# Optimization experiments

Measured on AMD Instinct MI355X. Metric: run time of the kernel, lower is better.

The kernel has to match this reference:

```python
import jax, jax.numpy as jnp
import numpy as np

N, C, T = 8, 256, 512
H, KQ, OUT = 8, 256, 256
EPS = 1e-5


def sym_linear(x, w, stride):
    # w: (2, out_dim); circulant-grouped expansion to (2T, out_dim), then x @ cp
    out_dim = w.shape[1]
    idx = (jnp.arange(out_dim)[None, :] - jnp.arange(T)[:, None] * stride) % out_dim  # (T, out_dim)
    cp = w[:, idx].transpose(1, 0, 2).reshape(2 * T, out_dim)  # cat of rolled copies
    return x @ cp


def ln2d(x, g, b):
    # LayerNorm over last two dims (T, 2T) with affine params (T, 2T)
    mu = jnp.mean(x, axis=(-2, -1), keepdims=True)
    var = jnp.mean(jnp.square(x - mu), axis=(-2, -1), keepdims=True)
    return (x - mu) / jnp.sqrt(var + EPS) * g + b


def setup_inputs() -> dict:
    key = jax.random.key(0)
    ks = jax.random.split(key, 16)
    stdv = 1.0 / np.sqrt(2 * T)
    u = lambda k, shape, s: jax.random.uniform(k, shape, jnp.float32, -s, s)
    return {
        "x": jax.random.normal(ks[0], (N, C, T), jnp.float32),
        "Wq": u(ks[1], (KQ, C), 1.0 / np.sqrt(C)),
        "Wk": u(ks[2], (KQ, C), 1.0 / np.sqrt(C)),
        "Wv": u(ks[3], (OUT, C), 1.0 / np.sqrt(C)),
        "m1w0": u(ks[4], (2, 2 * T), stdv),
        "m2w0": u(ks[5], (2, 2 * T), stdv),
        "m1w1": u(ks[6], (2, 2 * T), stdv),
        "m2w1": u(ks[7], (2, T), stdv),
        "ln1g0": 1.0 + 0.1 * jax.random.normal(ks[8], (T, 2 * T), jnp.float32),
        "ln1b0": 0.1 * jax.random.normal(ks[9], (T, 2 * T), jnp.float32),
        "ln2g0": 1.0 + 0.1 * jax.random.normal(ks[10], (T, 2 * T), jnp.float32),
        "ln2b0": 0.1 * jax.random.normal(ks[11], (T, 2 * T), jnp.float32),
        "ln1g1": 1.0 + 0.1 * jax.random.normal(ks[12], (T, 2 * T), jnp.float32),
        "ln1b1": 0.1 * jax.random.normal(ks[13], (T, 2 * T), jnp.float32),
    }


def reference(x, Wq, Wk, Wv, m1w0, m2w0, m1w1, m2w1,
              ln1g0, ln1b0, ln2g0, ln2b0, ln1g1, ln1b1):
    dk = KQ // H
    q = jnp.einsum('oc,nct->not', Wq, x).reshape(N, H, dk, T).transpose(0, 1, 3, 2)  # (N,H,T,dk)
    k = jnp.einsum('oc,nct->not', Wk, x).reshape(N, H, dk, T)                        # (N,H,dk,T)
    v = jnp.einsum('oc,nct->not', Wv, x).reshape(N, H, OUT // H, T).transpose(0, 1, 3, 2)  # (N,H,T,dv)

    scores = jnp.einsum('nhtd,nhds->nhts', q, k) / np.sqrt(dk)  # (N,H,T,T)
    ar = jnp.arange(T, dtype=jnp.float32)
    pd = jnp.abs(ar[None, :] - ar[:, None]) / (T - 1)  # (T,T)
    p = jnp.stack([scores, jnp.broadcast_to(pd, scores.shape)], axis=-1)  # (N,H,T,T,2)
    p = p.reshape(N, H, T, 2 * T)

    def transpose_pairs(z):
        return z.reshape(N, H, T, T, 2).transpose(0, 1, 3, 2, 4)

    # mix block 0 (intermediate)
    p = ln2d(sym_linear(p, m1w0, 2), ln1g0, ln1b0)
    p = jax.nn.gelu(transpose_pairs(p), approximate=False).reshape(N, H, T, 2 * T)
    p = ln2d(sym_linear(p, m2w0, 2), ln2g0, ln2b0)
    p = jax.nn.gelu(transpose_pairs(p), approximate=False).reshape(N, H, T, 2 * T)

    # mix block 1 (final)
    p = ln2d(sym_linear(p, m1w1, 2), ln1g1, ln1b1)
    p = jax.nn.gelu(transpose_pairs(p), approximate=False).reshape(N, H, T, 2 * T)
    p = sym_linear(p, m2w1, 1)           # (N,H,T,T), out_roll_stride = T // T * 1
    p = p.transpose(0, 1, 3, 2)

    attn = jax.nn.softmax(p, axis=-1)
    out = jnp.einsum('nhts,nhsd->nhtd', attn, v)  # (N,H,T,dv)
    return out.transpose(0, 1, 3, 2).reshape(N, OUT, T)
```

## Files before the change

### kernel.cpp

```cpp
#include <hip/hip_runtime.h>
#include <hip/hip_bf16.h>
#include <math.h>

#define CDIM 256
#define TDIM 512
#define T2   1024
#define NB   64
#define MTOT 524288.0f

typedef __bf16 bf16x8 __attribute__((ext_vector_type(8)));
typedef float  f32x4  __attribute__((ext_vector_type(4)));

__device__ __forceinline__ ushort f2bf(float f) {
  union { float f; unsigned u; } v; v.f = f;
  unsigned r = v.u + 0x7fffu + ((v.u >> 16) & 1u);
  return (ushort)(r >> 16);
}
__device__ __forceinline__ float bf2f(ushort h) {
  union { unsigned u; float f; } v; v.u = ((unsigned)h) << 16;
  return v.f;
}
__device__ __forceinline__ float gelu_exact(float x) {
  return 0.5f * x * (1.0f + erff(x * 0.7071067811865475f));
}

#define TO_LDS(p)  ((__attribute__((address_space(3))) void*)(unsigned)(uintptr_t)(p))
#define TO_GLB(p)  ((const __attribute__((address_space(1))) void*)(uintptr_t)(p))
#define GLOAD_LDS16(g, l) __builtin_amdgcn_global_load_lds(TO_GLB(g), TO_LDS(l), 16, 0, 0)

#define BAR()    asm volatile("s_barrier" ::: "memory")
#define WAITL()  asm volatile("s_waitcnt lgkmcnt(0)" ::: "memory")
#define WAITV4() asm volatile("s_waitcnt vmcnt(4)" ::: "memory")
#define WAITV0() asm volatile("s_waitcnt vmcnt(0)" ::: "memory")

__global__ __launch_bounds__(256)
void proj_kernel(const float* __restrict__ x, const float* __restrict__ Wq,
                 const float* __restrict__ Wk, const float* __restrict__ Wv,
                 float* __restrict__ qp, float* __restrict__ kp, float* __restrict__ vp) {
  int t = blockIdx.x * 256 + threadIdx.x;
  int o = blockIdx.y;
  int n = blockIdx.z;
  const float* xn = x + (long)n * CDIM * TDIM;
  float aq = 0.f, ak = 0.f, av = 0.f;
  for (int c = 0; c < CDIM; ++c) {
    float xv = xn[c * TDIM + t];
    aq = fmaf(Wq[o * CDIM + c], xv, aq);
    ak = fmaf(Wk[o * CDIM + c], xv, ak);
    av = fmaf(Wv[o * CDIM + c], xv, av);
  }
  long idx = ((long)n * 256 + o) * TDIM + t;
  qp[idx] = aq; kp[idx] = ak; vp[idx] = av;
}

__global__ __launch_bounds__(256)
void build_cpt_kernel(const float* __restrict__ w, ushort* __restrict__ cpt,
                      int outdim, int stride) {
  int i = blockIdx.x * 256 + threadIdx.x;
  int o  = i >> 10;
  int kk = i & 1023;
  int s = kk >> 1, r = kk & 1;
  float v = w[r * outdim + ((o - s * stride) & (outdim - 1))];
  cpt[i] = f2bf(v);
}

__global__ __launch_bounds__(256)
void build_p0_kernel(const float* __restrict__ qp, const float* __restrict__ kp,
                     ushort* __restrict__ P) {
  int s = blockIdx.x * 256 + threadIdx.x;
  int t = blockIdx.y;
  int b = blockIdx.z;
  int n = b >> 3, h = b & 7;
  const float* qrow = qp + ((long)n * 256 + h * 32) * TDIM + t;
  const float* krow = kp + ((long)n * 256 + h * 32) * TDIM + s;
  float acc = 0.f;
#pragma unroll
  for (int d = 0; d < 32; ++d) acc = fmaf(qrow[d * TDIM], krow[d * TDIM], acc);
  acc *= 0.17677669529663687f;
  float pd = fabsf((float)(s - t)) * (1.0f / 511.0f);
  ushort2 pr; pr.x = f2bf(acc); pr.y = f2bf(pd);
  *(ushort2*)(P + (((long)b * TDIM + t) * T2 + 2 * s)) = pr;
}


#define LDS_BUF  65536
#define LDS_BOFF 32768

#define STAGE_A_(buf, h, kt) do { \
  const ushort* gA0_ = Ab + (long)((h)*128 +      sr0) * 1024 + (kt)*64 + slog8; \
  const ushort* gA1_ = Ab + (long)((h)*128 + 64 + sr0) * 1024 + (kt)*64 + slog8; \
  char* dA_ = ldsw + (size_t)(buf) * LDS_BUF + (h)*16384 + tid*16; \
  GLOAD_LDS16(gA0_, dA_); GLOAD_LDS16(gA1_, dA_ + 8192); } while(0)

#define STAGE_B_(buf, h, kt) do { \
  const ushort* gB0_ = Bb + (long)((h)*128 +      sr0) * 1024 + (kt)*64 + slog8; \
  const ushort* gB1_ = Bb + (long)((h)*128 + 64 + sr0) * 1024 + (kt)*64 + slog8; \
  char* dB_ = ldsw + (size_t)(buf) * LDS_BUF + LDS_BOFF + (h)*16384 + tid*16; \
  GLOAD_LDS16(gB0_, dB_); GLOAD_LDS16(gB1_, dB_ + 8192); } while(0)

#define LD_A_(buf, mh) do { \
  const char* aB_ = ldsc + (size_t)(buf) * LDS_BUF; \
  _Pragma("unroll") for (int mi = 0; mi < 4; ++mi) { \
    int ar_ = wm*128 + (mh)*64 + mi*16 + fr; \
    const char* rb_ = aB_ + ar_*128; int sw_ = (ar_&7)<<4; \
    af[mi][0] = *(const bf16x8*)(rb_ + ((fq*16) ^ sw_)); \
    af[mi][1] = *(const bf16x8*)(rb_ + ((64 + fq*16) ^ sw_)); \
  } } while(0)

#define LD_B_(dst, buf, nh) do { \
  const char* bB_ = ldsc + (size_t)(buf) * LDS_BUF + LDS_BOFF; \
  _Pragma("unroll") for (int ni = 0; ni < 2; ++ni) { \
    int br_ = wn*64 + (nh)*32 + ni*16 + fr; \
    const char* rb_ = bB_ + br_*128; int sw_ = (br_&7)<<4; \
    dst[ni][0] = *(const bf16x8*)(rb_ + ((fq*16) ^ sw_)); \
    dst[ni][1] = *(const bf16x8*)(rb_ + ((64 + fq*16) ^ sw_)); \
  } } while(0)

#define QUAD_(mh, nh, bfa) do { \
  __builtin_amdgcn_s_setprio(1); \
  _Pragma("unroll") for (int kk = 0; kk < 2; ++kk) \
  _Pragma("unroll") for (int mi = 0; mi < 4; ++mi) \
  _Pragma("unroll") for (int ni = 0; ni < 2; ++ni) \
    acc[(mh)*4+mi][(nh)*2+ni] = __builtin_amdgcn_mfma_f32_16x16x32_bf16( \
        af[mi][kk], bfa[ni][kk], acc[(mh)*4+mi][(nh)*2+ni], 0, 0, 0); \
  __builtin_amdgcn_s_setprio(0); } while(0)

template<bool FINAL>
__global__ __launch_bounds__(512, 2)
void gemm256_kernel(const ushort* __restrict__ A, long aStride,
                    const ushort* __restrict__ BT, long bStride,
                    void* __restrict__ Out, int ncols, float* __restrict__ stats) {
  __shared__ ushort lds[2][2][256 * 64];
  const int tid = threadIdx.x;
  const int bm = blockIdx.x, bn = blockIdx.y, b = blockIdx.z;
  const ushort* Ab = A  + (long)b * aStride + (long)bm * 256 * 1024;
  const ushort* Bb = BT + (long)b * bStride + (long)bn * 256 * 1024;
  const int lane = tid & 63;
  const int fr = lane & 15, fq = lane >> 4;
  const int wid = tid >> 6, wm = wid >> 2, wn = wid & 3;
  const int sr0 = tid >> 3;
  const int slog8 = ((tid & 7) ^ (sr0 & 7)) * 8;
  const char* ldsc = (const char*)&lds[0][0][0];
  char*       ldsw = (char*)&lds[0][0][0];

  f32x4 acc[8][4] = {};
  bf16x8 af[4][2], bf0[2][2], bf1[2][2];

  STAGE_B_(0, 0, 0); STAGE_B_(0, 1, 0);
  STAGE_A_(0, 0, 0); STAGE_A_(0, 1, 0);
  STAGE_B_(1, 0, 1); STAGE_B_(1, 1, 1);
  WAITV4();
  BAR();

  for (int i = 0; i < 8; ++i) {
    const int t1 = 2 * i + 1, t2 = 2 * i + 2, t3 = 2 * i + 3;
    const bool st = (i < 7);
    LD_A_(0, 0); LD_B_(bf0, 0, 0);
    STAGE_A_(1, 0, t1);
    BAR(); WAITL(); QUAD_(0, 0, bf0); BAR();

    LD_B_(bf1, 0, 1);
    STAGE_A_(1, 1, t1);
    BAR(); WAITL(); QUAD_(0, 1, bf1); BAR();

    LD_A_(0, 1);
    if (st) STAGE_B_(0, 0, t2);
    BAR(); WAITL(); QUAD_(1, 1, bf1); BAR();

    if (st) { STAGE_B_(0, 1, t2); WAITV4(); } else { WAITV0(); }
    BAR(); QUAD_(1, 0, bf0); BAR();

    LD_A_(1, 0); LD_B_(bf0, 1, 0);
    if (st) STAGE_A_(0, 0, t2);
    BAR(); WAITL(); QUAD_(0, 0, bf0); BAR();

    LD_B_(bf1, 1, 1);
    if (st) STAGE_A_(0, 1, t2);
    BAR(); WAITL(); QUAD_(0, 1, bf1); BAR();

    LD_A_(1, 1);
    if (st) STAGE_B_(1, 0, t3);
    BAR(); WAITL(); QUAD_(1, 1, bf1); BAR();

    if (st) { STAGE_B_(1, 1, t3); WAITV4(); }
    BAR(); QUAD_(1, 0, bf0); BAR();
  }

  const int r0 = bm * 256 + wm * 128;
  const int c0 = bn * 256 + wn * 64;
  if (!FINAL) {
    ushort* Yb = (ushort*)Out + (long)b * 512 * ncols;
    float s1 = 0.f, s2 = 0.f;
#pragma unroll
    for (int mi = 0; mi < 8; ++mi)
#pragma unroll
      for (int ni = 0; ni < 4; ++ni)
#pragma unroll
        for (int r = 0; r < 4; ++r) {
          float v = acc[mi][ni][r];
          s1 += v; s2 += v * v;
          int row = r0 + mi * 16 + fq * 4 + r;
          int col = c0 + ni * 16 + fr;
          Yb[(long)row * ncols + col] = f2bf(v);
        }
    __syncthreads();
    float* red = (float*)&lds[0][0][0];
    red[tid] = s1; red[tid + 512] = s2;
    __syncthreads();
    for (int off = 256; off > 0; off >>= 1) {
      if (tid < off) { red[tid] += red[tid + off]; red[512 + tid] += red[512 + tid + off]; }
      __syncthreads();
    }
    if (tid == 0) {
      atomicAdd(&stats[b * 2],     red[0]);
      atomicAdd(&stats[b * 2 + 1], red[512]);
    }
  } else {
    float* Lb = (float*)Out + (long)b * 512 * 512;
#pragma unroll
    for (int mi = 0; mi < 8; ++mi)
#pragma unroll
      for (int ni = 0; ni < 4; ++ni)
#pragma unroll
        for (int r = 0; r < 4; ++r) {
          int row = r0 + mi * 16 + fq * 4 + r;
          int col = c0 + ni * 16 + fr;
          Lb[(long)row * 512 + col] = acc[mi][ni][r];
        }
  }
}

__global__ __launch_bounds__(256)
void apply_kernel(const ushort* __restrict__ Y, const float* __restrict__ stats,
                  const float* __restrict__ g, const float* __restrict__ bia,
                  ushort* __restrict__ P) {
  __shared__ ushort2 tile[32][33];
  int ti = blockIdx.x;
  int si = blockIdx.y;
  int b  = blockIdx.z;
  float mu  = stats[b * 2] * (1.0f / MTOT);
  float var = stats[b * 2 + 1] * (1.0f / MTOT) - mu * mu;
  float rstd = rsqrtf(var + 1e-5f);
  int tx = threadIdx.x & 31, ty = threadIdx.x >> 5;
  const ushort* Yb = Y + (long)b * 512 * 1024;
#pragma unroll
  for (int i = 0; i < 4; ++i) {
    int t  = ti * 32 + ty + i * 8;
    int sp = si * 32 + tx;
    ushort2 yv = *(const ushort2*)(Yb + (long)t * 1024 + 2 * sp);
    float2 gv = *(const float2*)(g   + (long)t * 1024 + 2 * sp);
    float2 bv = *(const float2*)(bia + (long)t * 1024 + 2 * sp);
    float y0 = (bf2f(yv.x) - mu) * rstd * gv.x + bv.x;
    float y1 = (bf2f(yv.y) - mu) * rstd * gv.y + bv.y;
    ushort2 o; o.x = f2bf(gelu_exact(y0)); o.y = f2bf(gelu_exact(y1));
    tile[ty + i * 8][tx] = o;
  }
  __syncthreads();
  ushort* Pb = P + (long)b * 512 * 1024;
#pragma unroll
  for (int i = 0; i < 4; ++i) {
    int srow = si * 32 + ty + i * 8;
    int tcol = ti * 32 + tx;
    ushort2 v = tile[tx][ty + i * 8];
    *(ushort2*)(Pb + (long)srow * 1024 + 2 * tcol) = v;
  }
}

__global__ __launch_bounds__(256)
void softmax_kernel(float* __restrict__ L) {
  int wid = threadIdx.x >> 6, lane = threadIdx.x & 63;
  long row = (long)blockIdx.x * 4 + wid;
  float* Lr = L + row * 512;
  float4 a = *(float4*)(Lr + lane * 8);
  float4 c = *(float4*)(Lr + lane * 8 + 4);
  float m = fmaxf(fmaxf(fmaxf(a.x, a.y), fmaxf(a.z, a.w)),
                  fmaxf(fmaxf(c.x, c.y), fmaxf(c.z, c.w)));
  for (int off = 32; off > 0; off >>= 1) m = fmaxf(m, __shfl_xor(m, off, 64));
  a.x = expf(a.x - m); a.y = expf(a.y - m); a.z = expf(a.z - m); a.w = expf(a.w - m);
  c.x = expf(c.x - m); c.y = expf(c.y - m); c.z = expf(c.z - m); c.w = expf(c.w - m);
  float s = a.x + a.y + a.z + a.w + c.x + c.y + c.z + c.w;
  for (int off = 32; off > 0; off >>= 1) s += __shfl_xor(s, off, 64);
  float inv = 1.0f / s;
  a.x *= inv; a.y *= inv; a.z *= inv; a.w *= inv;
  c.x *= inv; c.y *= inv; c.z *= inv; c.w *= inv;
  *(float4*)(Lr + lane * 8) = a;
  *(float4*)(Lr + lane * 8 + 4) = c;
}

__global__ __launch_bounds__(256)
void av_kernel(const float* __restrict__ L, const float* __restrict__ vp,
               float* __restrict__ out) {
  __shared__ float vt[32 * 512];
  int bh = blockIdx.x;
  int at = blockIdx.y;
  int n = bh >> 3, h = bh & 7;
  const float* vsrc = vp + ((long)n * 256 + h * 32) * 512;
  for (int i = threadIdx.x; i < 32 * 512 / 4; i += 256)
    ((float4*)vt)[i] = ((const float4*)vsrc)[i];
  __syncthreads();
  int a  = at * 32 + (threadIdx.x & 31);
  int d0 = (threadIdx.x >> 5) * 4;
  const float* Lr = L + ((long)bh * 512 + a) * 512;
  float acc0 = 0.f, acc1 = 0.f, acc2 = 0.f, acc3 = 0.f;
  for (int bcol = 0; bcol < 512; ++bcol) {
    float p = Lr[bcol];
    acc0 = fmaf(p, vt[(d0 + 0) * 512 + bcol], acc0);
    acc1 = fmaf(p, vt[(d0 + 1) * 512 + bcol], acc1);
    acc2 = fmaf(p, vt[(d0 + 2) * 512 + bcol], acc2);
    acc3 = fmaf(p, vt[(d0 + 3) * 512 + bcol], acc3);
  }
  float* ob = out + ((long)n * 256 + h * 32) * 512;
  ob[(d0 + 0) * 512 + a] = acc0;
  ob[(d0 + 1) * 512 + a] = acc1;
  ob[(d0 + 2) * 512 + a] = acc2;
  ob[(d0 + 3) * 512 + a] = acc3;
}

extern "C" void kernel_launch(void* const* d_in, const int* in_sizes, int n_in,
                              void* d_out, int out_size, void* d_ws, size_t ws_size,
                              hipStream_t stream) {
  const float* x     = (const float*)d_in[0];
  const float* Wq    = (const float*)d_in[1];
  const float* Wk    = (const float*)d_in[2];
  const float* Wv    = (const float*)d_in[3];
  const float* m1w0  = (const float*)d_in[4];
  const float* m2w0  = (const float*)d_in[5];
  const float* m1w1  = (const float*)d_in[6];
  const float* m2w1  = (const float*)d_in[7];
  const float* ln1g0 = (const float*)d_in[8];
  const float* ln1b0 = (const float*)d_in[9];
  const float* ln2g0 = (const float*)d_in[10];
  const float* ln2b0 = (const float*)d_in[11];
  const float* ln1g1 = (const float*)d_in[12];
  const float* ln1b1 = (const float*)d_in[13];

  char* w = (char*)d_ws;
  float*  qp    = (float*) (w + 0);
  float*  kp    = (float*) (w + (4ull  << 20));
  float*  vp    = (float*) (w + (8ull  << 20));
  float*  stats = (float*) (w + (12ull << 20));
  ushort* cpt0  = (ushort*)(w + (13ull << 20));
  ushort* cpt1  = (ushort*)(w + (15ull << 20));
  ushort* cpt2  = (ushort*)(w + (17ull << 20));
  ushort* cpt3  = (ushort*)(w + (19ull << 20));
  ushort* bufA  = (ushort*)(w + (20ull << 20));
  ushort* bufB  = (ushort*)(w + (84ull << 20));
  float*  L     = (float*)bufB;
  float*  outp  = (float*)d_out;

  hipMemsetAsync(stats, 0, 3 * NB * 2 * sizeof(float), stream);

  proj_kernel<<<dim3(2, 256, 8), 256, 0, stream>>>(x, Wq, Wk, Wv, qp, kp, vp);
  build_cpt_kernel<<<4096, 256, 0, stream>>>(m1w0, cpt0, 1024, 2);
  build_cpt_kernel<<<4096, 256, 0, stream>>>(m2w0, cpt1, 1024, 2);
  build_cpt_kernel<<<4096, 256, 0, stream>>>(m1w1, cpt2, 1024, 2);
  build_cpt_kernel<<<2048, 256, 0, stream>>>(m2w1, cpt3, 512, 1);
  build_p0_kernel<<<dim3(2, 512, 64), 256, 0, stream>>>(qp, kp, bufA);

  gemm256_kernel<false><<<dim3(2, 4, 64), 512, 0, stream>>>(bufA, 512L * 1024, cpt0, 0, bufB, 1024, stats);
  apply_kernel<<<dim3(16, 16, 64), 256, 0, stream>>>(bufB, stats, ln1g0, ln1b0, bufA);
  gemm256_kernel<false><<<dim3(2, 4, 64), 512, 0, stream>>>(bufA, 512L * 1024, cpt1, 0, bufB, 1024, stats + 128);
  apply_kernel<<<dim3(16, 16, 64), 256, 0, stream>>>(bufB, stats + 128, ln2g0, ln2b0, bufA);
  gemm256_kernel<false><<<dim3(2, 4, 64), 512, 0, stream>>>(bufA, 512L * 1024, cpt2, 0, bufB, 1024, stats + 256);
  apply_kernel<<<dim3(16, 16, 64), 256, 0, stream>>>(bufB, stats + 256, ln1g1, ln1b1, bufA);
  gemm256_kernel<true><<<dim3(2, 2, 64), 512, 0, stream>>>(cpt3, 0, bufA, 512L * 1024, L, 512, nullptr);
  softmax_kernel<<<8192, 256, 0, stream>>>(L);
  av_kernel<<<dim3(64, 16), 256, 0, stream>>>(L, vp, outp);
}
```

Baseline: 561.9 us.

## Split first mix GEMM into scores and shared positional parts; fuse softmax with AV

The interleaved (score, distance) input of the first mixing GEMM is split algebraically. The scores half is multiplied by the even-indexed circulant weights over K=512. The distance half is batch-independent, so it is computed once by a small GEMM and added in the epilogue. Scores are now computed with MFMA from bf16 q/k, weight prep kernels are merged into one launch, and softmax is fused into the AV kernel through an LDS tile. This removes half the K work of the first GEMM and an extra pass over L, at the cost of more code paths and a generalized K parameter in the GEMM.

```diff
diff --git a/kernel.cpp b/kernel.cpp
--- a/kernel.cpp
+++ b/kernel.cpp
@@ -36,7 +36,8 @@
 __global__ __launch_bounds__(256)
 void proj_kernel(const float* __restrict__ x, const float* __restrict__ Wq,
                  const float* __restrict__ Wk, const float* __restrict__ Wv,
-                 float* __restrict__ qp, float* __restrict__ kp, float* __restrict__ vp) {
+                 ushort* __restrict__ qb, ushort* __restrict__ kb,
+                 float* __restrict__ vp) {
   int t = blockIdx.x * 256 + threadIdx.x;
   int o = blockIdx.y;
   int n = blockIdx.z;
@@ -48,52 +49,78 @@
     ak = fmaf(Wk[o * CDIM + c], xv, ak);
     av = fmaf(Wv[o * CDIM + c], xv, av);
   }
-  long idx = ((long)n * 256 + o) * TDIM + t;
-  qp[idx] = aq; kp[idx] = ak; vp[idx] = av;
+  int h = o >> 5, d = o & 31;
+  long bidx = (((long)(n * 8 + h) * 512) + t) * 32 + d;
+  qb[bidx] = f2bf(aq);
+  kb[bidx] = f2bf(ak);
+  vp[((long)n * 256 + o) * TDIM + t] = av;
 }
 
 __global__ __launch_bounds__(256)
-void build_cpt_kernel(const float* __restrict__ w, ushort* __restrict__ cpt,
-                      int outdim, int stride) {
-  int i = blockIdx.x * 256 + threadIdx.x;
-  int o  = i >> 10;
-  int kk = i & 1023;
-  int s = kk >> 1, r = kk & 1;
-  float v = w[r * outdim + ((o - s * stride) & (outdim - 1))];
-  cpt[i] = f2bf(v);
+void prep_kernel(const float* __restrict__ m1w0, const float* __restrict__ m2w0,
+                 const float* __restrict__ m1w1, const float* __restrict__ m2w1,
+                 ushort* __restrict__ cpte0, ushort* __restrict__ cpto0,
+                 ushort* __restrict__ cpt1, ushort* __restrict__ cpt2,
+                 ushort* __restrict__ cpt3, ushort* __restrict__ pdb) {
+  long i = (long)blockIdx.x * 256 + threadIdx.x;
+  if (i < 524288) {
+    int o = (int)(i >> 9), s = (int)(i & 511);
+    int idx = (o - 2 * s) & 1023;
+    cpte0[i] = f2bf(m1w0[idx]);
+    cpto0[i] = f2bf(m1w0[1024 + idx]);
+  } else if (i < 1572864) {
+    long j = i - 524288;
+    int o = (int)(j >> 10), kk = (int)(j & 1023);
+    cpt1[j] = f2bf(m2w0[(kk & 1) * 1024 + ((o - 2 * (kk >> 1)) & 1023)]);
+  } else if (i < 2621440) {
+    long j = i - 1572864;
+    int o = (int)(j >> 10), kk = (int)(j & 1023);
+    cpt2[j] = f2bf(m1w1[(kk & 1) * 1024 + ((o - 2 * (kk >> 1)) & 1023)]);
+  } else if (i < 3145728) {
+    long j = i - 2621440;
+    int o = (int)(j >> 10), kk = (int)(j & 1023);
+    cpt3[j] = f2bf(m2w1[(kk & 1) * 512 + ((o - (kk >> 1)) & 511)]);
+  } else if (i < 3407872) {
+    long j = i - 3145728;
+    int t = (int)(j >> 9), s = (int)(j & 511);
+    pdb[j] = f2bf(fabsf((float)(s - t)) * (1.0f / 511.0f));
+  }
 }
 
 __global__ __launch_bounds__(256)
-void build_p0_kernel(const float* __restrict__ qp, const float* __restrict__ kp,
-                     ushort* __restrict__ P) {
-  int s = blockIdx.x * 256 + threadIdx.x;
-  int t = blockIdx.y;
-  int b = blockIdx.z;
-  int n = b >> 3, h = b & 7;
-  const float* qrow = qp + ((long)n * 256 + h * 32) * TDIM + t;
-  const float* krow = kp + ((long)n * 256 + h * 32) * TDIM + s;
-  float acc = 0.f;
-#pragma unroll
-  for (int d = 0; d < 32; ++d) acc = fmaf(qrow[d * TDIM], krow[d * TDIM], acc);
-  acc *= 0.17677669529663687f;
-  float pd = fabsf((float)(s - t)) * (1.0f / 511.0f);
-  ushort2 pr; pr.x = f2bf(acc); pr.y = f2bf(pd);
-  *(ushort2*)(P + (((long)b * TDIM + t) * T2 + 2 * s)) = pr;
-}
-
+void scores_kernel(const ushort* __restrict__ qb, const ushort* __restrict__ kb,
+                   ushort* __restrict__ S) {
+  int tb = blockIdx.x;
+  int b  = blockIdx.y;
+  int wv = threadIdx.x >> 6, lane = threadIdx.x & 63;
+  int fr = lane & 15, fq = lane >> 4;
+  int t0 = tb * 64 + wv * 16;
+  bf16x8 af = *(const bf16x8*)(qb + ((long)b * 512 + t0 + fr) * 32 + fq * 8);
+  const ushort* kbase = kb + (long)b * 512 * 32 + fr * 32 + fq * 8;
+  ushort* Sb = S + ((long)b * 512 + t0 + fq * 4) * 512 + fr;
+  f32x4 zz = {0.f, 0.f, 0.f, 0.f};
+#pragma unroll 4
+  for (int st = 0; st < 32; ++st) {
+    bf16x8 bfv = *(const bf16x8*)(kbase + st * 512);
+    f32x4 acc = __builtin_amdgcn_mfma_f32_16x16x32_bf16(af, bfv, zz, 0, 0, 0);
+#pragma unroll
+    for (int r = 0; r < 4; ++r)
+      Sb[(long)r * 512 + st * 16] = f2bf(acc[r] * 0.17677669529663687f);
+  }
+}
 
 #define LDS_BUF  65536
 #define LDS_BOFF 32768
 
 #define STAGE_A_(buf, h, kt) do { \
-  const ushort* gA0_ = Ab + (long)((h)*128 +      sr0) * 1024 + (kt)*64 + slog8; \
-  const ushort* gA1_ = Ab + (long)((h)*128 + 64 + sr0) * 1024 + (kt)*64 + slog8; \
+  const ushort* gA0_ = Ab + (long)((h)*128 +      sr0) * Krow + (kt)*64 + slog8; \
+  const ushort* gA1_ = Ab + (long)((h)*128 + 64 + sr0) * Krow + (kt)*64 + slog8; \
   char* dA_ = ldsw + (size_t)(buf) * LDS_BUF + (h)*16384 + tid*16; \
   GLOAD_LDS16(gA0_, dA_); GLOAD_LDS16(gA1_, dA_ + 8192); } while(0)
 
 #define STAGE_B_(buf, h, kt) do { \
-  const ushort* gB0_ = Bb + (long)((h)*128 +      sr0) * 1024 + (kt)*64 + slog8; \
-  const ushort* gB1_ = Bb + (long)((h)*128 + 64 + sr0) * 1024 + (kt)*64 + slog8; \
+  const ushort* gB0_ = Bb + (long)((h)*128 +      sr0) * Krow + (kt)*64 + slog8; \
+  const ushort* gB1_ = Bb + (long)((h)*128 + 64 + sr0) * Krow + (kt)*64 + slog8; \
   char* dB_ = ldsw + (size_t)(buf) * LDS_BUF + LDS_BOFF + (h)*16384 + tid*16; \
   GLOAD_LDS16(gB0_, dB_); GLOAD_LDS16(gB1_, dB_ + 8192); } while(0)
 
@@ -128,12 +155,15 @@
 __global__ __launch_bounds__(512, 2)
 void gemm256_kernel(const ushort* __restrict__ A, long aStride,
                     const ushort* __restrict__ BT, long bStride,
-                    void* __restrict__ Out, int ncols, float* __restrict__ stats) {
+                    void* __restrict__ Out, int ncols, float* __restrict__ stats,
+                    const float* __restrict__ Cadd, int K) {
   __shared__ ushort lds[2][2][256 * 64];
   const int tid = threadIdx.x;
   const int bm = blockIdx.x, bn = blockIdx.y, b = blockIdx.z;
-  const ushort* Ab = A  + (long)b * aStride + (long)bm * 256 * 1024;
-  const ushort* Bb = BT + (long)b * bStride + (long)bn * 256 * 1024;
+  const int Krow = K;
+  const int nkt2 = K >> 7;
+  const ushort* Ab = A  + (long)b * aStride + (long)bm * 256 * Krow;
+  const ushort* Bb = BT + (long)b * bStride + (long)bn * 256 * Krow;
   const int lane = tid & 63;
   const int fr = lane & 15, fq = lane >> 4;
   const int wid = tid >> 6, wm = wid >> 2, wn = wid & 3;
@@ -151,9 +181,9 @@
   WAITV4();
   BAR();
 
-  for (int i = 0; i < 8; ++i) {
+  for (int i = 0; i < nkt2; ++i) {
     const int t1 = 2 * i + 1, t2 = 2 * i + 2, t3 = 2 * i + 3;
-    const bool st = (i < 7);
+    const bool st = (i < nkt2 - 1);
     LD_A_(0, 0); LD_B_(bf0, 0, 0);
     STAGE_A_(1, 0, t1);
     BAR(); WAITL(); QUAD_(0, 0, bf0); BAR();
@@ -197,9 +227,10 @@
 #pragma unroll
         for (int r = 0; r < 4; ++r) {
           float v = acc[mi][ni][r];
-          s1 += v; s2 += v * v;
           int row = r0 + mi * 16 + fq * 4 + r;
           int col = c0 + ni * 16 + fr;
+          if (Cadd) v += Cadd[(long)row * ncols + col];
+          s1 += v; s2 += v * v;
           Yb[(long)row * ncols + col] = f2bf(v);
         }
     __syncthreads();
@@ -215,7 +246,7 @@
       atomicAdd(&stats[b * 2 + 1], red[512]);
     }
   } else {
-    float* Lb = (float*)Out + (long)b * 512 * 512;
+    float* Lb = (float*)Out + (long)b * 512 * ncols;
 #pragma unroll
     for (int mi = 0; mi < 8; ++mi)
 #pragma unroll
@@ -224,7 +255,7 @@
         for (int r = 0; r < 4; ++r) {
           int row = r0 + mi * 16 + fq * 4 + r;
           int col = c0 + ni * 16 + fr;
-          Lb[(long)row * 512 + col] = acc[mi][ni][r];
+          Lb[(long)row * ncols + col] = acc[mi][ni][r];
         }
   }
 }
@@ -266,53 +297,54 @@
 }
 
 __global__ __launch_bounds__(256)
-void softmax_kernel(float* __restrict__ L) {
-  int wid = threadIdx.x >> 6, lane = threadIdx.x & 63;
-  long row = (long)blockIdx.x * 4 + wid;
-  float* Lr = L + row * 512;
-  float4 a = *(float4*)(Lr + lane * 8);
-  float4 c = *(float4*)(Lr + lane * 8 + 4);
-  float m = fmaxf(fmaxf(fmaxf(a.x, a.y), fmaxf(a.z, a.w)),
-                  fmaxf(fmaxf(c.x, c.y), fmaxf(c.z, c.w)));
-  for (int off = 32; off > 0; off >>= 1) m = fmaxf(m, __shfl_xor(m, off, 64));
-  a.x = expf(a.x - m); a.y = expf(a.y - m); a.z = expf(a.z - m); a.w = expf(a.w - m);
-  c.x = expf(c.x - m); c.y = expf(c.y - m); c.z = expf(c.z - m); c.w = expf(c.w - m);
-  float s = a.x + a.y + a.z + a.w + c.x + c.y + c.z + c.w;
-  for (int off = 32; off > 0; off >>= 1) s += __shfl_xor(s, off, 64);
-  float inv = 1.0f / s;
-  a.x *= inv; a.y *= inv; a.z *= inv; a.w *= inv;
-  c.x *= inv; c.y *= inv; c.z *= inv; c.w *= inv;
-  *(float4*)(Lr + lane * 8) = a;
-  *(float4*)(Lr + lane * 8 + 4) = c;
-}
-
-__global__ __launch_bounds__(256)
-void av_kernel(const float* __restrict__ L, const float* __restrict__ vp,
-               float* __restrict__ out) {
-  __shared__ float vt[32 * 512];
+void smax_av_kernel(const float* __restrict__ L, const float* __restrict__ vp,
+                    float* __restrict__ out) {
+  __shared__ float Lt[32][513];
   int bh = blockIdx.x;
   int at = blockIdx.y;
   int n = bh >> 3, h = bh & 7;
-  const float* vsrc = vp + ((long)n * 256 + h * 32) * 512;
-  for (int i = threadIdx.x; i < 32 * 512 / 4; i += 256)
-    ((float4*)vt)[i] = ((const float4*)vsrc)[i];
+  int wv = threadIdx.x >> 6, lane = threadIdx.x & 63;
+  for (int rr = 0; rr < 8; ++rr) {
+    int row = wv * 8 + rr;
+    int a = at * 32 + row;
+    const float* Lr = L + ((long)bh * 512 + a) * 512;
+    float e[8];
+#pragma unroll
+    for (int j = 0; j < 8; ++j) e[j] = Lr[j * 64 + lane];
+    float m = e[0];
+#pragma unroll
+    for (int j = 1; j < 8; ++j) m = fmaxf(m, e[j]);
+    for (int off = 32; off > 0; off >>= 1) m = fmaxf(m, __shfl_xor(m, off, 64));
+    float s = 0.f;
+#pragma unroll
+    for (int j = 0; j < 8; ++j) { e[j] = expf(e[j] - m); s += e[j]; }
+    for (int off = 32; off > 0; off >>= 1) s += __shfl_xor(s, off, 64);
+    float inv = 1.0f / s;
+#pragma unroll
+    for (int j = 0; j < 8; ++j) Lt[row][j * 64 + lane] = e[j] * inv;
+  }
   __syncthreads();
-  int a  = at * 32 + (threadIdx.x & 31);
+  int r  = threadIdx.x & 31;
   int d0 = (threadIdx.x >> 5) * 4;
-  const float* Lr = L + ((long)bh * 512 + a) * 512;
-  float acc0 = 0.f, acc1 = 0.f, acc2 = 0.f, acc3 = 0.f;
-  for (int bcol = 0; bcol < 512; ++bcol) {
-    float p = Lr[bcol];
-    acc0 = fmaf(p, vt[(d0 + 0) * 512 + bcol], acc0);
-    acc1 = fmaf(p, vt[(d0 + 1) * 512 + bcol], acc1);
-    acc2 = fmaf(p, vt[(d0 + 2) * 512 + bcol], acc2);
-    acc3 = fmaf(p, vt[(d0 + 3) * 512 + bcol], acc3);
-  }
+  const float* vb = vp + ((long)n * 256 + h * 32) * 512;
+  float a0 = 0.f, a1 = 0.f, a2 = 0.f, a3 = 0.f;
+  for (int bc = 0; bc < 512; bc += 4) {
+    float4 v0 = *(const float4*)(vb + (d0 + 0) * 512 + bc);
+    float4 v1 = *(const float4*)(vb + (d0 + 1) * 512 + bc);
+    float4 v2 = *(const float4*)(vb + (d0 + 2) * 512 + bc);
+    float4 v3 = *(const float4*)(vb + (d0 + 3) * 512 + bc);
+    float p0 = Lt[r][bc], p1 = Lt[r][bc + 1], p2 = Lt[r][bc + 2], p3 = Lt[r][bc + 3];
+    a0 = fmaf(p0, v0.x, fmaf(p1, v0.y, fmaf(p2, v0.z, fmaf(p3, v0.w, a0))));
+    a1 = fmaf(p0, v1.x, fmaf(p1, v1.y, fmaf(p2, v1.z, fmaf(p3, v1.w, a1))));
+    a2 = fmaf(p0, v2.x, fmaf(p1, v2.y, fmaf(p2, v2.z, fmaf(p3, v2.w, a2))));
+    a3 = fmaf(p0, v3.x, fmaf(p1, v3.y, fmaf(p2, v3.z, fmaf(p3, v3.w, a3))));
+  }
+  int a = at * 32 + r;
   float* ob = out + ((long)n * 256 + h * 32) * 512;
-  ob[(d0 + 0) * 512 + a] = acc0;
-  ob[(d0 + 1) * 512 + a] = acc1;
-  ob[(d0 + 2) * 512 + a] = acc2;
-  ob[(d0 + 3) * 512 + a] = acc3;
+  ob[(d0 + 0) * 512 + a] = a0;
+  ob[(d0 + 1) * 512 + a] = a1;
+  ob[(d0 + 2) * 512 + a] = a2;
+  ob[(d0 + 3) * 512 + a] = a3;
 }
 
 extern "C" void kernel_launch(void* const* d_in, const int* in_sizes, int n_in,
@@ -334,35 +366,41 @@
   const float* ln1b1 = (const float*)d_in[13];
 
   char* w = (char*)d_ws;
-  float*  qp    = (float*) (w + 0);
-  float*  kp    = (float*) (w + (4ull  << 20));
-  float*  vp    = (float*) (w + (8ull  << 20));
-  float*  stats = (float*) (w + (12ull << 20));
-  ushort* cpt0  = (ushort*)(w + (13ull << 20));
-  ushort* cpt1  = (ushort*)(w + (15ull << 20));
-  ushort* cpt2  = (ushort*)(w + (17ull << 20));
-  ushort* cpt3  = (ushort*)(w + (19ull << 20));
-  ushort* bufA  = (ushort*)(w + (20ull << 20));
-  ushort* bufB  = (ushort*)(w + (84ull << 20));
-  float*  L     = (float*)bufB;
-  float*  outp  = (float*)d_out;
+  float*  vp     = (float*) (w + 0);
+  ushort* qb     = (ushort*)(w + (4ull  << 20));
+  ushort* kb     = (ushort*)(w + (6ull  << 20));
+  float*  stats  = (float*) (w + (8ull  << 20));
+  ushort* cpte0  = (ushort*)(w + (9ull  << 20));
+  ushort* cpto0  = (ushort*)(w + (10ull << 20));
+  ushort* cpt1   = (ushort*)(w + (11ull << 20));
+  ushort* cpt2   = (ushort*)(w + (13ull << 20));
+  ushort* cpt3   = (ushort*)(w + (15ull << 20));
+  ushort* pdb    = (ushort*)(w + (16ull << 20));
+  float*  pdpart = (float*) (w + (17ull << 20));
+  ushort* bufA   = (ushort*)(w + (20ull << 20));
+  ushort* bufB   = (ushort*)(w + (84ull << 20));
+  ushort* S      = bufA;
+  float*  L      = (float*)bufB;
+  float*  outp   = (float*)d_out;
 
   hipMemsetAsync(stats, 0, 3 * NB * 2 * sizeof(float), stream);
 
-  proj_kernel<<<dim3(2, 256, 8), 256, 0, stream>>>(x, Wq, Wk, Wv, qp, kp, vp);
-  build_cpt_kernel<<<4096, 256, 0, stream>>>(m1w0, cpt0, 1024, 2);
-  build_cpt_kernel<<<4096, 256, 0, stream>>>(m2w0, cpt1, 1024, 2);
-  build_cpt_kernel<<<4096, 256, 0, stream>>>(m1w1, cpt2, 1024, 2);
-  build_cpt_kernel<<<2048, 256, 0, stream>>>(m2w1, cpt3, 512, 1);
-  build_p0_kernel<<<dim3(2, 512, 64), 256, 0, stream>>>(qp, kp, bufA);
-
-  gemm256_kernel<false><<<dim3(2, 4, 64), 512, 0, stream>>>(bufA, 512L * 1024, cpt0, 0, bufB, 1024, stats);
+  proj_kernel<<<dim3(2, 256, 8), 256, 0, stream>>>(x, Wq, Wk, Wv, qb, kb, vp);
+  prep_kernel<<<13312, 256, 0, stream>>>(m1w0, m2w0, m1w1, m2w1,
+                                         cpte0, cpto0, cpt1, cpt2, cpt3, pdb);
+  scores_kernel<<<dim3(8, 64), 256, 0, stream>>>(qb, kb, S);
+  gemm256_kernel<true><<<dim3(2, 4, 1), 512, 0, stream>>>(
+      pdb, 0, cpto0, 0, pdpart, 1024, nullptr, nullptr, 512);
+  gemm256_kernel<false><<<dim3(2, 4, 64), 512, 0, stream>>>(
+      S, 512L * 512, cpte0, 0, bufB, 1024, stats, pdpart, 512);
   apply_kernel<<<dim3(16, 16, 64), 256, 0, stream>>>(bufB, stats, ln1g0, ln1b0, bufA);
-  gemm256_kernel<false><<<dim3(2, 4, 64), 512, 0, stream>>>(bufA, 512L * 1024, cpt1, 0, bufB, 1024, stats + 128);
+  gemm256_kernel<false><<<dim3(2, 4, 64), 512, 0, stream>>>(
+      bufA, 512L * 1024, cpt1, 0, bufB, 1024, stats + 128, nullptr, 1024);
   apply_kernel<<<dim3(16, 16, 64), 256, 0, stream>>>(bufB, stats + 128, ln2g0, ln2b0, bufA);
-  gemm256_kernel<false><<<dim3(2, 4, 64), 512, 0, stream>>>(bufA, 512L * 1024, cpt2, 0, bufB, 1024, stats + 256);
+  gemm256_kernel<false><<<dim3(2, 4, 64), 512, 0, stream>>>(
+      bufA, 512L * 1024, cpt2, 0, bufB, 1024, stats + 256, nullptr, 1024);
   apply_kernel<<<dim3(16, 16, 64), 256, 0, stream>>>(bufB, stats + 256, ln1g1, ln1b1, bufA);
-  gemm256_kernel<true><<<dim3(2, 2, 64), 512, 0, stream>>>(cpt3, 0, bufA, 512L * 1024, L, 512, nullptr);
-  softmax_kernel<<<8192, 256, 0, stream>>>(L);
-  av_kernel<<<dim3(64, 16), 256, 0, stream>>>(L, vp, outp);
-}
+  gemm256_kernel<true><<<dim3(2, 2, 64), 512, 0, stream>>>(
+      cpt3, 0, bufA, 512L * 1024, L, 512, nullptr, nullptr, 1024);
+  smax_av_kernel<<<dim3(64, 16), 256, 0, stream>>>(L, vp, outp);
+}
```

Result: faster. 528.1 us (-6.0%).
